# Kernel tuning notes

Measured on AMD Instinct MI355X. Metric: run time of the kernel, lower is better.

The kernel has to match this reference:

```python
import jax, jax.numpy as jnp
import numpy as np
from jax import lax

DG = 8  # deformable groups


def conv3(x, w, b):
    # 3x3 stride-1 SAME conv, NCHW/OIHW
    y = lax.conv_general_dilated(x, w, (1, 1), 'SAME',
                                 dimension_numbers=('NCHW', 'OIHW', 'NCHW'))
    return y + b[None, :, None, None]


def lrelu(x):
    return jnp.where(x >= 0, x, 0.1 * x)


def _mdcn(x, offset, mask, w, b, dg):
    """Modulated deformable conv v2: 3x3, stride 1, pad 1, dilation 1, groups 1.
    offset: [B, 2*dg*9, H, W] (first dg*9 = y offsets, second dg*9 = x offsets),
    mask:   [B, dg*9, H, W] (already sigmoided)."""
    B, C, H, W = x.shape
    kk = 9
    Cg = C // dg
    off = offset.reshape(B, 2, dg, kk, H, W)
    oy, ox = off[:, 0], off[:, 1]            # [B, dg, kk, H, W]
    m = mask.reshape(B, dg, kk, H, W)
    ky = (jnp.arange(kk) // 3 - 1).astype(x.dtype).reshape(1, 1, kk, 1, 1)
    kx = (jnp.arange(kk) % 3 - 1).astype(x.dtype).reshape(1, 1, kk, 1, 1)
    hg = jnp.arange(H, dtype=x.dtype).reshape(1, 1, 1, H, 1)
    wg = jnp.arange(W, dtype=x.dtype).reshape(1, 1, 1, 1, W)
    py = hg + ky + oy                        # sampling positions (pad=1 cancels k-1 shift)
    px = wg + kx + ox
    y0 = jnp.floor(py)
    x0 = jnp.floor(px)
    wy = py - y0
    wx = px - x0
    xg = x.reshape(B, dg, Cg, H * W)
    acc = jnp.zeros((B, dg, Cg, kk, H, W), x.dtype)
    for dy, dx, wgt in ((0.0, 0.0, (1 - wy) * (1 - wx)),
                        (0.0, 1.0, (1 - wy) * wx),
                        (1.0, 0.0, wy * (1 - wx)),
                        (1.0, 1.0, wy * wx)):
        yy = y0 + dy
        xx = x0 + dx
        valid = (yy >= 0) & (yy < H) & (xx >= 0) & (xx < W)
        yi = jnp.clip(yy, 0, H - 1).astype(jnp.int32)
        xi = jnp.clip(xx, 0, W - 1).astype(jnp.int32)
        idx = (yi * W + xi).reshape(B, dg, 1, kk * H * W)
        v = jnp.take_along_axis(xg, idx, axis=3).reshape(B, dg, Cg, kk, H, W)
        acc = acc + v * (wgt * valid.astype(x.dtype))[:, :, None]
    acc = acc * m[:, :, None]                # modulation mask
    sampled = acc.reshape(B, C, kk, H, W)
    out = jnp.einsum('bckhw,ock->bohw', sampled, w.reshape(w.shape[0], C, kk))
    return out + b[None, :, None, None]


def _dcn_pack(x, feat, w_om, b_om, w, b):
    out = conv3(feat, w_om, b_om)            # [B, 3*dg*9, H, W]
    o1, o2, mr = jnp.split(out, 3, axis=1)
    offset = jnp.concatenate([o1, o2], axis=1)
    mask = jax.nn.sigmoid(mr)
    return _mdcn(x, offset, mask, w, b, DG)


def _forward(ref, neb,
             w_oc1, b_oc1, w_om1, b_om1, w_dcn1, b_dcn1, w_fc, b_fc,
             w_cas1, b_cas1, w_cas2, b_cas2, w_om2, b_om2, w_dcn2, b_dcn2,
             w_ta1, b_ta1, w_ta2, b_ta2, w_ff, b_ff):
    start = ref
    # --- PCD alignment (nbr_feat_l = neb, ref_feat_l = ref) ---
    off = lrelu(conv3(jnp.concatenate([neb, ref], axis=1), w_oc1, b_oc1))
    feat = _dcn_pack(neb, off, w_om1, b_om1, w_dcn1, b_dcn1)
    feat = lrelu(conv3(feat, w_fc, b_fc))
    off = jnp.concatenate([feat, ref], axis=1)
    off = lrelu(conv3(lrelu(conv3(off, w_cas1, b_cas1)), w_cas2, b_cas2))
    feat = lrelu(_dcn_pack(feat, off, w_om2, b_om2, w_dcn2, b_dcn2))
    # --- TSA fusion (ref=ref, neb=feat) ---
    emb_ref = conv3(ref, w_ta1, b_ta1)
    emb = conv3(feat, w_ta2, b_ta2)
    corr = jnp.sum(emb * emb_ref, axis=1, keepdims=True)  # [B,1,H,W]
    feat = lrelu(conv3(ref * corr, w_ff, b_ff))
    return feat + start


def setup_inputs() -> dict:
    key = jax.random.key(0)
    ks = jax.random.split(key, 32)
    B, C, H, W = 4, 64, 180, 320
    s = 0.05
    p = lambda k, shape: (jax.random.normal(k, shape, jnp.float32) * s)
    OM = 3 * DG * 9  # 216
    return {
        'ref': jax.random.normal(ks[0], (B, C, H, W), jnp.float32),
        'neb': jax.random.normal(ks[1], (B, C, H, W), jnp.float32),
        'w_oc1': p(ks[2], (C, 2 * C, 3, 3)), 'b_oc1': p(ks[3], (C,)),
        'w_om1': p(ks[4], (OM, C, 3, 3)),    'b_om1': p(ks[5], (OM,)),
        'w_dcn1': p(ks[6], (C, C, 3, 3)),    'b_dcn1': p(ks[7], (C,)),
        'w_fc': p(ks[8], (C, C, 3, 3)),      'b_fc': p(ks[9], (C,)),
        'w_cas1': p(ks[10], (C, 2 * C, 3, 3)), 'b_cas1': p(ks[11], (C,)),
        'w_cas2': p(ks[12], (C, C, 3, 3)),   'b_cas2': p(ks[13], (C,)),
        'w_om2': p(ks[14], (OM, C, 3, 3)),   'b_om2': p(ks[15], (OM,)),
        'w_dcn2': p(ks[16], (C, C, 3, 3)),   'b_dcn2': p(ks[17], (C,)),
        'w_ta1': p(ks[18], (C, C, 3, 3)),    'b_ta1': p(ks[19], (C,)),
        'w_ta2': p(ks[20], (C, C, 3, 3)),    'b_ta2': p(ks[21], (C,)),
        'w_ff': p(ks[22], (C, C, 3, 3)),     'b_ff': p(ks[23], (C,)),
    }


def reference(ref, neb,
              w_oc1, b_oc1, w_om1, b_om1, w_dcn1, b_dcn1, w_fc, b_fc,
              w_cas1, b_cas1, w_cas2, b_cas2, w_om2, b_om2, w_dcn2, b_dcn2,
              w_ta1, b_ta1, w_ta2, b_ta2, w_ff, b_ff):
    return _forward(ref, neb,
                    w_oc1, b_oc1, w_om1, b_om1, w_dcn1, b_dcn1, w_fc, b_fc,
                    w_cas1, b_cas1, w_cas2, b_cas2, w_om2, b_om2, w_dcn2, b_dcn2,
                    w_ta1, b_ta1, w_ta2, b_ta2, w_ff, b_ff)
```

## Files before the change

### kernel.cpp

```cpp
#include <hip/hip_runtime.h>
#include <cmath>


using short8 = __attribute__((ext_vector_type(8))) short;
using f32x4  = __attribute__((ext_vector_type(4))) float;
using f32x2  = __attribute__((ext_vector_type(2))) float;

#define DEVINL static __device__ __forceinline__

DEVINL unsigned short f2bf(float f){
    unsigned u = __float_as_uint(f);
    u += 0x7fffu + ((u >> 16) & 1u);
    return (unsigned short)(u >> 16);
}
DEVINL unsigned pack2(float a, float b){ return (unsigned)f2bf(a) | ((unsigned)f2bf(b) << 16); }
DEVINL float bflo(unsigned u){ return __uint_as_float(u << 16); }
DEVINL float bfhi(unsigned u){ return __uint_as_float(u & 0xffff0000u); }
DEVINL float bf2f(unsigned short u){ return __uint_as_float((unsigned)u << 16); }
DEVINL float lrelu_f(float v){ return v >= 0.f ? v : 0.1f * v; }
DEVINL f32x2 up2(unsigned u){
    return f32x2{__uint_as_float(u << 16), __uint_as_float(u & 0xffff0000u)};
}

DEVINL void swz_decode(int& bx, int& by, int& bz){
    const int gx = gridDim.x, gy = gridDim.y;
    int lin = blockIdx.x + gx * (blockIdx.y + gy * blockIdx.z);
    int nwg = gx * gy * gridDim.z;
    int q = nwg >> 3, r = nwg & 7;
    int xcd = lin & 7, idx = lin >> 3;
    int swz = (xcd < r ? xcd * (q + 1) : r + xcd * q) + idx;
    bz = swz / (gx * gy);
    int rem = swz - bz * gx * gy;
    by = rem / gx; bx = rem - by * gx;
}

struct Ptr4 { unsigned short* p[4]; };

__global__ __launch_bounds__(256) void nchw2nhwc2(const float* __restrict__ inA,
                                                  const float* __restrict__ inB,
                                                  unsigned short* __restrict__ outA,
                                                  unsigned short* __restrict__ outB)
{
    constexpr int HW = 180 * 320;
    const int blk = blockIdx.x;
    const float* in = (blk < 900) ? inA : inB;
    unsigned short* out = (blk < 900) ? outA : outB;
    size_t idx = (size_t)(blk % 900) * 256 + threadIdx.x;
    size_t bb = idx / HW, p = idx % HW;
    const float* src = in + (bb * 64) * (size_t)HW + p;
    unsigned short* dst = out + idx * 64;
    #pragma unroll
    for (int c0 = 0; c0 < 64; c0 += 16) {
        unsigned r[8];
        #pragma unroll
        for (int q = 0; q < 8; ++q)
            r[q] = pack2(src[(size_t)(c0 + 2*q) * HW], src[(size_t)(c0 + 2*q + 1) * HW]);
        *(uint4*)(dst + c0)     = *(uint4*)&r[0];
        *(uint4*)(dst + c0 + 8) = *(uint4*)&r[4];
    }
}

struct PrepArgs {
    const float* src[11];
    unsigned short* dst[11];
    int cout[11]; int cin[11]; int nch[11]; int kind[11];
};

__global__ __launch_bounds__(256) void prep_all(PrepArgs a)
{
    const int t = blockIdx.y;
    const int idx = blockIdx.x * 256 + threadIdx.x;
    if (a.kind[t] == 1) {
        if (idx >= 36864) return;
        int kk = idx & 31, oc = (idx >> 5) & 63, s = idx >> 11;
        int k = s * 32 + kk;
        int gt = k >> 3, c8 = k & 7;
        int tap = gt >> 3, g = gt & 7;
        a.dst[t][idx] = f2bf(a.src[t][((size_t)oc * 64 + g * 8 + c8) * 9 + tap]);
    } else {
        int cin = a.cin[t], cout = a.cout[t];
        int ncs = cin / 32;
        int total = a.nch[t] * 9 * ncs * 2048;
        if (idx >= total) return;
        int kk = idx & 31, oc_l = (idx >> 5) & 63, rest = idx >> 11;
        int cs = rest % ncs; int rest2 = rest / ncs;
        int j = rest2 % 9; int ch = rest2 / 9;
        int oc = ch * 64 + oc_l, c = cs * 32 + kk;
        float v = (oc < cout) ? a.src[t][((size_t)oc * cin + c) * 9 + j] : 0.f;
        a.dst[t][idx] = f2bf(v);
    }
}

template<int CIN, bool TWO_IN, bool ACT, bool SCALE, int OUTMODE, int NM, int NF>
__global__ __launch_bounds__(256, (CIN == 128 ? 2 : 3)) void conv_mfma(
    const unsigned short* __restrict__ in0, const unsigned short* __restrict__ in1,
    const unsigned short* __restrict__ wgt, const float* __restrict__ bias,
    unsigned short* __restrict__ out, const float* __restrict__ corr,
    const float* __restrict__ res, float* __restrict__ outf,
    Ptr4 omout, int choff, int zdiv, int COUT)
{
    constexpr int H = 180, W = 320, HW = H * W;
    constexpr int NCB = CIN / 8;
    constexpr int NCS = CIN / 32;
    constexpr int XW  = NF * 16 + 2;
    __shared__ __align__(16) unsigned char lds[6 * XW * CIN * 2];

    const int tid = threadIdx.x;
    int bx, by, bz;
    swz_decode(bx, by, bz);
    int b, ch;
    if (OUTMODE == 1) { b = bz / zdiv; ch = bz % zdiv + choff; }
    else              { b = bz; ch = 0; }
    const int x0 = bx * (NF * 16), y0 = by * 4;

    for (int t = tid; t < 6 * XW * NCB; t += 256) {
        int cb = t % NCB; int r = t / NCB;
        int xp = r % XW, yp = r / XW;
        int gx = x0 - 1 + xp, gy = y0 - 1 + yp;
        uint4 v = make_uint4(0, 0, 0, 0);
        if (gx >= 0 && gx < W && gy >= 0 && gy < H) {
            size_t pix = (size_t)b * HW + (size_t)gy * W + gx;
            const unsigned short* src;
            if (TWO_IN) src = (cb < 8) ? (in0 + pix * 64 + cb * 8) : (in1 + pix * 64 + (cb - 8) * 8);
            else        src = in0 + pix * CIN + cb * 8;
            v = *(const uint4*)src;
            if (SCALE) {
                float cv = corr[pix];
                v.x = pack2(bflo(v.x) * cv, bfhi(v.x) * cv);
                v.y = pack2(bflo(v.y) * cv, bfhi(v.y) * cv);
                v.z = pack2(bflo(v.z) * cv, bfhi(v.z) * cv);
                v.w = pack2(bflo(v.w) * cv, bfhi(v.w) * cv);
            }
        }
        int blk = cb ^ (xp & 7);
        *(uint4*)&lds[(size_t)((yp * XW + xp) * NCB + blk) * 16] = v;
    }
    __syncthreads();

    const int wv = tid >> 6, lane = tid & 63;
    const int ll = lane & 15, lh = lane >> 4;
    const unsigned short* wchunk = wgt + (size_t)ch * (9 * NCS * 2048);
    const int alane = ll * 32 + lh * 8;

    f32x4 acc[NM][NF];
    #pragma unroll
    for (int mi = 0; mi < NM; ++mi)
        #pragma unroll
        for (int nf = 0; nf < NF; ++nf) acc[mi][nf] = f32x4{0.f, 0.f, 0.f, 0.f};

    #pragma unroll
    for (int j = 0; j < 9; ++j) {
        const int jy = j / 3, jx = j % 3;
        #pragma unroll
        for (int cs = 0; cs < NCS; ++cs) {
            const int s = j * NCS + cs;
            short8 a[NM];
            #pragma unroll
            for (int mi = 0; mi < NM; ++mi)
                a[mi] = *(const short8*)(wchunk + (size_t)s * 2048 + mi * 512 + alane);
            short8 bf[NF];
            #pragma unroll
            for (int nf = 0; nf < NF; ++nf) {
                int xp = nf * 16 + ll + jx;
                int blk = (cs * 4 + lh) ^ (xp & 7);
                int addr = (((wv + jy) * XW + xp) * NCB + blk) * 16;
                bf[nf] = *(const short8*)&lds[addr];
            }
            #pragma unroll
            for (int mi = 0; mi < NM; ++mi)
                #pragma unroll
                for (int nf = 0; nf < NF; ++nf)
                    acc[mi][nf] = __builtin_amdgcn_mfma_f32_16x16x32_bf16(a[mi], bf[nf], acc[mi][nf], 0, 0, 0);
        }
    }

    const int py = y0 + wv;
    const size_t pixrow = (size_t)b * HW + (size_t)py * W;
    #pragma unroll
    for (int nf = 0; nf < NF; ++nf) {
        const int px = x0 + nf * 16 + ll;
        if (OUTMODE == 1) {
            unsigned short* oslot = omout.p[b];
            #pragma unroll
            for (int mi = 0; mi < NM; ++mi) {
                const int oc_l = mi * 16 + lh * 4;
                #pragma unroll
                for (int jj = 0; jj < 4; ++jj) {
                    int ocg = ch * 64 + oc_l + jj;
                    if (ocg < COUT) {
                        float t = acc[mi][nf][jj] + bias[ocg];
                        oslot[(size_t)ocg * HW + (size_t)py * W + px] = f2bf(ACT ? lrelu_f(t) : t);
                    }
                }
            }
        } else {
            #pragma unroll
            for (int mi = 0; mi < NM; ++mi) {
                const int oc_l = mi * 16 + lh * 4;
                if (OUTMODE == 0) {
                    float v[4];
                    #pragma unroll
                    for (int jj = 0; jj < 4; ++jj) {
                        float t = acc[mi][nf][jj] + bias[oc_l + jj];
                        v[jj] = ACT ? lrelu_f(t) : t;
                    }
                    uint2 st; st.x = pack2(v[0], v[1]); st.y = pack2(v[2], v[3]);
                    *(uint2*)&out[(pixrow + px) * 64 + oc_l] = st;
                } else {
                    #pragma unroll
                    for (int jj = 0; jj < 4; ++jj) {
                        int oc = oc_l + jj;
                        float t = acc[mi][nf][jj] + bias[oc];
                        if (ACT) t = lrelu_f(t);
                        size_t idx = ((size_t)b * 64 + oc) * HW + (size_t)py * W + px;
                        outf[idx] = t + res[idx];
                    }
                }
            }
        }
    }
}

__global__ __launch_bounds__(256, 3) void tacorr_mfma(
    const unsigned short* __restrict__ inR,
    const unsigned short* __restrict__ inE,
    const unsigned short* __restrict__ wR, const float* __restrict__ bR,
    const unsigned short* __restrict__ wE, const float* __restrict__ bE,
    float* __restrict__ outf)
{
    constexpr int H = 180, W = 320, HW = H * W;
    constexpr int NE1 = 6 * 34 * 8;
    __shared__ __align__(16) unsigned char lds[2][6 * 34 * 64 * 2];

    const int tid = threadIdx.x;
    int bx, by, bz;
    swz_decode(bx, by, bz);
    const int b = bz;
    const int x0 = bx * 32, y0 = by * 4;

    for (int t = tid; t < 2 * NE1; t += 256) {
        int half = t / NE1, e = t - half * NE1;
        int cb = e & 7; int r = e >> 3;
        int xp = r % 34, yp = r / 34;
        int gx = x0 - 1 + xp, gy = y0 - 1 + yp;
        uint4 v = make_uint4(0, 0, 0, 0);
        if (gx >= 0 && gx < W && gy >= 0 && gy < H) {
            size_t pix = (size_t)b * HW + (size_t)gy * W + gx;
            const unsigned short* src = (half ? inE : inR) + pix * 64 + cb * 8;
            v = *(const uint4*)src;
        }
        int blk = cb ^ (xp & 7);
        *(uint4*)&lds[half][(size_t)((yp * 34 + xp) * 8 + blk) * 16] = v;
    }
    __syncthreads();

    const int wv = tid >> 6, lane = tid & 63;
    const int ll = lane & 15, lh = lane >> 4;
    const int alane = ll * 32 + lh * 8;

    f32x4 accR[4][2], accE[4][2];
    #pragma unroll
    for (int mi = 0; mi < 4; ++mi)
        #pragma unroll
        for (int nf = 0; nf < 2; ++nf) { accR[mi][nf] = f32x4{0,0,0,0}; accE[mi][nf] = f32x4{0,0,0,0}; }

    #pragma unroll
    for (int j = 0; j < 9; ++j) {
        const int jy = j / 3, jx = j % 3;
        #pragma unroll
        for (int cs = 0; cs < 2; ++cs) {
            const int s = j * 2 + cs;
            short8 aR[4], aE[4];
            #pragma unroll
            for (int mi = 0; mi < 4; ++mi) {
                aR[mi] = *(const short8*)(wR + (size_t)s * 2048 + mi * 512 + alane);
                aE[mi] = *(const short8*)(wE + (size_t)s * 2048 + mi * 512 + alane);
            }
            #pragma unroll
            for (int nf = 0; nf < 2; ++nf) {
                int xp = nf * 16 + ll + jx;
                int blk = (cs * 4 + lh) ^ (xp & 7);
                int addr = (((wv + jy) * 34 + xp) * 8 + blk) * 16;
                short8 bfR = *(const short8*)&lds[0][addr];
                short8 bfE = *(const short8*)&lds[1][addr];
                #pragma unroll
                for (int mi = 0; mi < 4; ++mi) {
                    accR[mi][nf] = __builtin_amdgcn_mfma_f32_16x16x32_bf16(aR[mi], bfR, accR[mi][nf], 0, 0, 0);
                    accE[mi][nf] = __builtin_amdgcn_mfma_f32_16x16x32_bf16(aE[mi], bfE, accE[mi][nf], 0, 0, 0);
                }
            }
        }
    }

    const int py = y0 + wv;
    const size_t pixrow = (size_t)b * HW + (size_t)py * W;
    #pragma unroll
    for (int nf = 0; nf < 2; ++nf) {
        const int px = x0 + nf * 16 + ll;
        float dot = 0.f;
        #pragma unroll
        for (int mi = 0; mi < 4; ++mi) {
            const int oc_l = mi * 16 + lh * 4;
            #pragma unroll
            for (int jj = 0; jj < 4; ++jj)
                dot += (accR[mi][nf][jj] + bR[oc_l + jj]) * (accE[mi][nf][jj] + bE[oc_l + jj]);
        }
        dot += __shfl_xor(dot, 16);
        dot += __shfl_xor(dot, 32);
        if (lh == 0) outf[pixrow + px] = dot;
    }
}

template<int ACT>
__global__ __launch_bounds__(256, 6) void mdcn_mfma(
    const unsigned short* __restrict__ x, Ptr4 omslots,
    const unsigned short* __restrict__ wgt, const float* __restrict__ bias,
    unsigned short* __restrict__ out)
{
    constexpr int H = 180, W = 320, HW = H * W;
    constexpr size_t CHW = (size_t)HW * 64;
    __shared__ __align__(16) unsigned char sv[40 * 32 * 16];

    const int tid = threadIdx.x;
    int bx, by, bz;
    swz_decode(bx, by, bz);
    const unsigned short* xb  = x + (size_t)bz * CHW;
    const unsigned short* omb = omslots.p[bz];
    unsigned short* ob        = out + (size_t)bz * CHW;
    const int px0 = bx * 32;
    const int py  = by;

    const int pxl = tid & 31, g = tid >> 5;
    const int px = px0 + pxl;
    const size_t p = (size_t)py * W + px;
    const unsigned short* omg = omb + (size_t)(g * 9) * HW + p;

    float oyv[9], oxv[9], mmv[9];
    #pragma unroll
    for (int k = 0; k < 9; ++k) oyv[k] = bf2f(omg[(size_t)k * HW]);
    #pragma unroll
    for (int k = 0; k < 9; ++k) oxv[k] = bf2f(omg[(size_t)(72 + k) * HW]);
    #pragma unroll
    for (int k = 0; k < 9; ++k) mmv[k] = bf2f(omg[(size_t)(144 + k) * HW]);

    auto SAMPLE = [&](int k, int row){
        float m = 1.f / (1.f + __expf(-mmv[k]));
        float pyf = (float)(py + (k / 3) - 1) + oyv[k];
        float pxf = (float)(px + (k % 3) - 1) + oxv[k];
        float y0f = floorf(pyf), x0f = floorf(pxf);
        float wy = pyf - y0f, wx = pxf - x0f;
        int yi = (int)y0f, xi = (int)x0f;
        bool vy0 = (yi >= 0) && (yi < H);
        bool vy1 = (yi + 1 >= 0) && (yi + 1 < H);
        bool vx0 = (xi >= 0) && (xi < W);
        bool vx1 = (xi + 1 >= 0) && (xi + 1 < W);
        float w00 = (vy0 && vx0) ? (1.f - wy) * (1.f - wx) * m : 0.f;
        float w01 = (vy0 && vx1) ? (1.f - wy) * wx * m : 0.f;
        float w10 = (vy1 && vx0) ? wy * (1.f - wx) * m : 0.f;
        float w11 = (vy1 && vx1) ? wy * wx * m : 0.f;
        int yc0 = min(max(yi, 0), H - 1), yc1 = min(max(yi + 1, 0), H - 1);
        int xc0 = min(max(xi, 0), W - 1), xc1 = min(max(xi + 1, 0), W - 1);
        uint4 c00 = *(const uint4*)(xb + ((size_t)(yc0 * W + xc0) * 64 + g * 8));
        uint4 c01 = *(const uint4*)(xb + ((size_t)(yc0 * W + xc1) * 64 + g * 8));
        uint4 c10 = *(const uint4*)(xb + ((size_t)(yc1 * W + xc0) * 64 + g * 8));
        uint4 c11 = *(const uint4*)(xb + ((size_t)(yc1 * W + xc1) * 64 + g * 8));
        const unsigned* p00 = (const unsigned*)&c00;
        const unsigned* p01 = (const unsigned*)&c01;
        const unsigned* p10 = (const unsigned*)&c10;
        const unsigned* p11 = (const unsigned*)&c11;
        unsigned r[4];
        #pragma unroll
        for (int q = 0; q < 4; ++q) {
            f32x2 rv = up2(p00[q]) * w00 + up2(p01[q]) * w01
                     + up2(p10[q]) * w10 + up2(p11[q]) * w11;
            r[q] = pack2(rv[0], rv[1]);
        }
        *(uint4*)&sv[(size_t)(row * 32 + pxl) * 16] = *(uint4*)r;
    };

    const int wv = tid >> 6, lane = tid & 63;
    const int ll = lane & 15, lh = lane >> 4;
    f32x4 acc[2] = {f32x4{0.f,0.f,0.f,0.f}, f32x4{0.f,0.f,0.f,0.f}};

    #pragma unroll
    for (int k = 0; k < 5; ++k) SAMPLE(k, k * 8 + g);
    __syncthreads();
    #pragma unroll
    for (int s = 0; s < 10; ++s) {
        short8 a = *(const short8*)(wgt + (size_t)(s * 64 + wv * 16 + ll) * 32 + lh * 8);
        #pragma unroll
        for (int nf = 0; nf < 2; ++nf) {
            short8 bb = *(const short8*)&sv[(size_t)s * 2048 + lh * 512 + (nf * 16 + ll) * 16];
            acc[nf] = __builtin_amdgcn_mfma_f32_16x16x32_bf16(a, bb, acc[nf], 0, 0, 0);
        }
    }
    __syncthreads();
    #pragma unroll
    for (int k = 5; k < 9; ++k) SAMPLE(k, (k - 5) * 8 + g);
    __syncthreads();
    #pragma unroll
    for (int s = 0; s < 8; ++s) {
        short8 a = *(const short8*)(wgt + (size_t)((10 + s) * 64 + wv * 16 + ll) * 32 + lh * 8);
        #pragma unroll
        for (int nf = 0; nf < 2; ++nf) {
            short8 bb = *(const short8*)&sv[(size_t)s * 2048 + lh * 512 + (nf * 16 + ll) * 16];
            acc[nf] = __builtin_amdgcn_mfma_f32_16x16x32_bf16(a, bb, acc[nf], 0, 0, 0);
        }
    }

    #pragma unroll
    for (int nf = 0; nf < 2; ++nf) {
        int opx = px0 + nf * 16 + ll;
        int oc0 = wv * 16 + lh * 4;
        float v[4];
        #pragma unroll
        for (int jj = 0; jj < 4; ++jj) {
            float t = acc[nf][jj] + bias[oc0 + jj];
            v[jj] = ACT ? lrelu_f(t) : t;
        }
        uint2 st; st.x = pack2(v[0], v[1]); st.y = pack2(v[2], v[3]);
        *(uint2*)&ob[((size_t)py * W + opx) * 64 + oc0] = st;
    }
}

extern "C" void kernel_launch(void* const* d_in, const int* in_sizes, int n_in,
                              void* d_out, int out_size, void* d_ws, size_t ws_size,
                              hipStream_t stream)
{
    const float* ref    = (const float*)d_in[0];
    const float* neb    = (const float*)d_in[1];
    const float* w_oc1  = (const float*)d_in[2];  const float* b_oc1  = (const float*)d_in[3];
    const float* w_om1  = (const float*)d_in[4];  const float* b_om1  = (const float*)d_in[5];
    const float* w_dcn1 = (const float*)d_in[6];  const float* b_dcn1 = (const float*)d_in[7];
    const float* w_fc   = (const float*)d_in[8];  const float* b_fc   = (const float*)d_in[9];
    const float* w_cas1 = (const float*)d_in[10]; const float* b_cas1 = (const float*)d_in[11];
    const float* w_cas2 = (const float*)d_in[12]; const float* b_cas2 = (const float*)d_in[13];
    const float* w_om2  = (const float*)d_in[14]; const float* b_om2  = (const float*)d_in[15];
    const float* w_dcn2 = (const float*)d_in[16]; const float* b_dcn2 = (const float*)d_in[17];
    const float* w_ta1  = (const float*)d_in[18]; const float* b_ta1  = (const float*)d_in[19];
    const float* w_ta2  = (const float*)d_in[20]; const float* b_ta2  = (const float*)d_in[21];
    const float* w_ff   = (const float*)d_in[22]; const float* b_ff   = (const float*)d_in[23];

    constexpr int H = 180, W = 320, HW = H * W;
    constexpr size_t CHW = (size_t)HW * 64;
    constexpr size_t SLB = 4 * CHW * 2;
    constexpr size_t OMSLOT_EL = (size_t)HW * 216;
    constexpr size_t OMSLOT_B  = OMSLOT_EL * 2;

    char* wsb = (char*)d_ws;
    unsigned short* S0 = (unsigned short*)(wsb);
    unsigned short* S1 = (unsigned short*)(wsb + SLB);
    unsigned short* S2 = (unsigned short*)(wsb + 2 * SLB);
    unsigned short* S3 = (unsigned short*)(wsb + 3 * SLB);
    float* corrf = (float*)S3;
    unsigned short* ffw = (unsigned short*)(wsb + SLB + (2u << 20));

    char* doutb = (char*)d_out;
    unsigned short* omA0 = (unsigned short*)doutb;
    unsigned short* omA1 = omA0 + OMSLOT_EL;
    unsigned short* wb   = (unsigned short*)(doutb + 2 * OMSLOT_B);
    const bool big = ws_size >= 4 * SLB + 2 * OMSLOT_B;
    unsigned short* omB0 = (unsigned short*)(wsb + 4 * SLB);
    unsigned short* omB1 = omB0 + OMSLOT_EL;

    unsigned short* w_oc1p = wb + 0;
    unsigned short* w_om1p = wb + 73728;
    unsigned short* w_dcn1p= wb + 221184;
    unsigned short* w_fcp  = wb + 258048;
    unsigned short* w_cas1p= wb + 294912;
    unsigned short* w_cas2p= wb + 368640;
    unsigned short* w_om2p = wb + 405504;
    unsigned short* w_dcn2p= wb + 552960;
    unsigned short* w_ta1p = wb + 589824;
    unsigned short* w_ta2p = wb + 626688;
    unsigned short* w_ffp  = wb + 663552;

    dim3 blk(256);
    dim3 g4(10, 45, 4);
    dim3 g4w(5, 45, 4);
    Ptr4 none{};

    nchw2nhwc2<<<1800, blk, 0, stream>>>(ref, neb, S0, S1);

    {
        PrepArgs pa;
        const float* srcs[11] = {w_oc1, w_om1, w_dcn1, w_fc, w_cas1, w_cas2, w_om2, w_dcn2, w_ta1, w_ta2, w_ff};
        unsigned short* dsts[11] = {w_oc1p, w_om1p, w_dcn1p, w_fcp, w_cas1p, w_cas2p, w_om2p, w_dcn2p, w_ta1p, w_ta2p, w_ffp};
        int couts[11] = {64, 216, 0, 64, 64, 64, 216, 0, 64, 64, 64};
        int cins[11]  = {128, 64, 0, 64, 128, 64, 64, 0, 64, 64, 64};
        int nchs[11]  = {1, 4, 0, 1, 1, 1, 4, 0, 1, 1, 1};
        int kinds[11] = {0, 0, 1, 0, 0, 0, 0, 1, 0, 0, 0};
        for (int i = 0; i < 11; ++i) {
            pa.src[i] = srcs[i]; pa.dst[i] = dsts[i];
            pa.cout[i] = couts[i]; pa.cin[i] = cins[i]; pa.nch[i] = nchs[i]; pa.kind[i] = kinds[i];
        }
        prep_all<<<dim3(576, 11), blk, 0, stream>>>(pa);
    }

    conv_mfma<128, true, true, false, 0, 4, 2><<<g4, blk, 0, stream>>>(
        S1, S0, w_oc1p, b_oc1, S2, nullptr, nullptr, nullptr, none, 0, 1, 64);

    auto ompack = [&](const unsigned short* inp, const unsigned short* wp, const float* bp,
                      Ptr4 slots, int nb){
        conv_mfma<64, false, false, false, 1, 4, 4><<<dim3(5, 45, 3 * nb), blk, 0, stream>>>(
            inp, nullptr, wp, bp, nullptr, nullptr, nullptr, nullptr, slots, 0, 3, 216);
        conv_mfma<64, false, false, false, 1, 2, 4><<<dim3(5, 45, nb), blk, 0, stream>>>(
            inp, nullptr, wp, bp, nullptr, nullptr, nullptr, nullptr, slots, 3, 1, 216);
    };

    if (big) {
        Ptr4 slots{omA0, omA1, omB0, omB1};
        ompack(S2, w_om1p, b_om1, slots, 4);
        mdcn_mfma<0><<<dim3(10, 180, 4), blk, 0, stream>>>(S1, slots, w_dcn1p, b_dcn1, S3);
    } else {
        Ptr4 slots{omA0, omA1, nullptr, nullptr};
        for (int pp = 0; pp < 2; ++pp) {
            ompack(S2 + 2 * pp * CHW, w_om1p, b_om1, slots, 2);
            mdcn_mfma<0><<<dim3(10, 180, 2), blk, 0, stream>>>(S1 + 2 * pp * CHW, slots,
                                                               w_dcn1p, b_dcn1, S3 + 2 * pp * CHW);
        }
    }

    conv_mfma<64, false, true, false, 0, 4, 4><<<g4w, blk, 0, stream>>>(
        S3, nullptr, w_fcp, b_fc, S2, nullptr, nullptr, nullptr, none, 0, 1, 64);
    conv_mfma<128, true, true, false, 0, 4, 2><<<g4, blk, 0, stream>>>(
        S2, S0, w_cas1p, b_cas1, S1, nullptr, nullptr, nullptr, none, 0, 1, 64);
    conv_mfma<64, false, true, false, 0, 4, 4><<<g4w, blk, 0, stream>>>(
        S1, nullptr, w_cas2p, b_cas2, S3, nullptr, nullptr, nullptr, none, 0, 1, 64);

    if (big) {
        Ptr4 slots{omA0, omA1, omB0, omB1};
        ompack(S3, w_om2p, b_om2, slots, 4);
        mdcn_mfma<1><<<dim3(10, 180, 4), blk, 0, stream>>>(S2, slots, w_dcn2p, b_dcn2, S1);
    } else {
        Ptr4 slots{omA0, omA1, nullptr, nullptr};
        for (int pp = 0; pp < 2; ++pp) {
            ompack(S3 + 2 * pp * CHW, w_om2p, b_om2, slots, 2);
            mdcn_mfma<1><<<dim3(10, 180, 2), blk, 0, stream>>>(S2 + 2 * pp * CHW, slots,
                                                               w_dcn2p, b_dcn2, S1 + 2 * pp * CHW);
        }
    }

    tacorr_mfma<<<g4, blk, 0, stream>>>(S0, S1, w_ta1p, b_ta1, w_ta2p, b_ta2, corrf);

    hipMemcpyAsync(ffw, w_ffp, 36864 * 2, hipMemcpyDeviceToDevice, stream);

    conv_mfma<64, false, true, true, 2, 4, 4><<<g4w, blk, 0, stream>>>(
        S0, nullptr, ffw, b_ff, nullptr, corrf, ref, (float*)d_out, none, 0, 1, 64);
}
```

Before: 1.161 ms.

## Double mdcn block to 512 threads, sampling all nine taps in one phase

The deformable-conv kernel now runs 512 threads per block. The two halves of the block sample taps 0-4 and 5-8 at the same time into a larger shared buffer (72 rows instead of 40), with a single barrier before the MFMA phase. Each of the 8 waves then computes one 16x16 output tile over all 18 K-steps, instead of 4 waves each doing two tiles in two phases. This removes two barriers and the serial sample-compute-sample sequence and exposes more gather parallelism. In exchange it uses more LDS per block and tighter register limits under launch_bounds(512,8), which may reduce the number of resident blocks.

```diff
diff --git a/kernel.cpp b/kernel.cpp
--- a/kernel.cpp
+++ b/kernel.cpp
@@ -312,14 +312,14 @@
 }
 
 template<int ACT>
-__global__ __launch_bounds__(256, 6) void mdcn_mfma(
+__global__ __launch_bounds__(512, 8) void mdcn_mfma(
     const unsigned short* __restrict__ x, Ptr4 omslots,
     const unsigned short* __restrict__ wgt, const float* __restrict__ bias,
     unsigned short* __restrict__ out)
 {
     constexpr int H = 180, W = 320, HW = H * W;
     constexpr size_t CHW = (size_t)HW * 64;
-    __shared__ __align__(16) unsigned char sv[40 * 32 * 16];
+    __shared__ __align__(16) unsigned char sv[72 * 32 * 16];
 
     const int tid = threadIdx.x;
     int bx, by, bz;
@@ -330,23 +330,15 @@
     const int px0 = bx * 32;
     const int py  = by;
 
-    const int pxl = tid & 31, g = tid >> 5;
+    const int pxl = tid & 31, g = (tid >> 5) & 7, hh = tid >> 8;
     const int px = px0 + pxl;
     const size_t p = (size_t)py * W + px;
     const unsigned short* omg = omb + (size_t)(g * 9) * HW + p;
 
-    float oyv[9], oxv[9], mmv[9];
-    #pragma unroll
-    for (int k = 0; k < 9; ++k) oyv[k] = bf2f(omg[(size_t)k * HW]);
-    #pragma unroll
-    for (int k = 0; k < 9; ++k) oxv[k] = bf2f(omg[(size_t)(72 + k) * HW]);
-    #pragma unroll
-    for (int k = 0; k < 9; ++k) mmv[k] = bf2f(omg[(size_t)(144 + k) * HW]);
-
-    auto SAMPLE = [&](int k, int row){
-        float m = 1.f / (1.f + __expf(-mmv[k]));
-        float pyf = (float)(py + (k / 3) - 1) + oyv[k];
-        float pxf = (float)(px + (k % 3) - 1) + oxv[k];
+    auto SAMPLE = [&](int k, float oy, float ox, float mr){
+        float m = 1.f / (1.f + __expf(-mr));
+        float pyf = (float)(py + (k / 3) - 1) + oy;
+        float pxf = (float)(px + (k % 3) - 1) + ox;
         float y0f = floorf(pyf), x0f = floorf(pxf);
         float wy = pyf - y0f, wx = pxf - x0f;
         int yi = (int)y0f, xi = (int)x0f;
@@ -375,47 +367,50 @@
                      + up2(p10[q]) * w10 + up2(p11[q]) * w11;
             r[q] = pack2(rv[0], rv[1]);
         }
-        *(uint4*)&sv[(size_t)(row * 32 + pxl) * 16] = *(uint4*)r;
+        *(uint4*)&sv[(size_t)((k * 8 + g) * 32 + pxl) * 16] = *(uint4*)r;
     };
+
+    if (hh == 0) {
+        float oy[5], ox[5], mr[5];
+        #pragma unroll
+        for (int k = 0; k < 5; ++k) oy[k] = bf2f(omg[(size_t)k * HW]);
+        #pragma unroll
+        for (int k = 0; k < 5; ++k) ox[k] = bf2f(omg[(size_t)(72 + k) * HW]);
+        #pragma unroll
+        for (int k = 0; k < 5; ++k) mr[k] = bf2f(omg[(size_t)(144 + k) * HW]);
+        #pragma unroll
+        for (int k = 0; k < 5; ++k) SAMPLE(k, oy[k], ox[k], mr[k]);
+    } else {
+        float oy[4], ox[4], mr[4];
+        #pragma unroll
+        for (int k = 0; k < 4; ++k) oy[k] = bf2f(omg[(size_t)(5 + k) * HW]);
+        #pragma unroll
+        for (int k = 0; k < 4; ++k) ox[k] = bf2f(omg[(size_t)(77 + k) * HW]);
+        #pragma unroll
+        for (int k = 0; k < 4; ++k) mr[k] = bf2f(omg[(size_t)(149 + k) * HW]);
+        #pragma unroll
+        for (int k = 0; k < 4; ++k) SAMPLE(5 + k, oy[k], ox[k], mr[k]);
+    }
+    __syncthreads();
 
     const int wv = tid >> 6, lane = tid & 63;
     const int ll = lane & 15, lh = lane >> 4;
-    f32x4 acc[2] = {f32x4{0.f,0.f,0.f,0.f}, f32x4{0.f,0.f,0.f,0.f}};
-
-    #pragma unroll
-    for (int k = 0; k < 5; ++k) SAMPLE(k, k * 8 + g);
-    __syncthreads();
-    #pragma unroll
-    for (int s = 0; s < 10; ++s) {
-        short8 a = *(const short8*)(wgt + (size_t)(s * 64 + wv * 16 + ll) * 32 + lh * 8);
-        #pragma unroll
-        for (int nf = 0; nf < 2; ++nf) {
-            short8 bb = *(const short8*)&sv[(size_t)s * 2048 + lh * 512 + (nf * 16 + ll) * 16];
-            acc[nf] = __builtin_amdgcn_mfma_f32_16x16x32_bf16(a, bb, acc[nf], 0, 0, 0);
-        }
-    }
-    __syncthreads();
-    #pragma unroll
-    for (int k = 5; k < 9; ++k) SAMPLE(k, (k - 5) * 8 + g);
-    __syncthreads();
-    #pragma unroll
-    for (int s = 0; s < 8; ++s) {
-        short8 a = *(const short8*)(wgt + (size_t)((10 + s) * 64 + wv * 16 + ll) * 32 + lh * 8);
-        #pragma unroll
-        for (int nf = 0; nf < 2; ++nf) {
-            short8 bb = *(const short8*)&sv[(size_t)s * 2048 + lh * 512 + (nf * 16 + ll) * 16];
-            acc[nf] = __builtin_amdgcn_mfma_f32_16x16x32_bf16(a, bb, acc[nf], 0, 0, 0);
-        }
-    }
-
-    #pragma unroll
-    for (int nf = 0; nf < 2; ++nf) {
+    const int og = wv & 3, nf = wv >> 2;
+    f32x4 acc = f32x4{0.f, 0.f, 0.f, 0.f};
+    #pragma unroll
+    for (int s = 0; s < 18; ++s) {
+        short8 a = *(const short8*)(wgt + (size_t)(s * 64 + og * 16 + ll) * 32 + lh * 8);
+        short8 bb = *(const short8*)&sv[(size_t)s * 2048 + lh * 512 + (nf * 16 + ll) * 16];
+        acc = __builtin_amdgcn_mfma_f32_16x16x32_bf16(a, bb, acc, 0, 0, 0);
+    }
+
+    {
         int opx = px0 + nf * 16 + ll;
-        int oc0 = wv * 16 + lh * 4;
+        int oc0 = og * 16 + lh * 4;
         float v[4];
         #pragma unroll
         for (int jj = 0; jj < 4; ++jj) {
-            float t = acc[nf][jj] + bias[oc0 + jj];
+            float t = acc[jj] + bias[oc0 + jj];
             v[jj] = ACT ? lrelu_f(t) : t;
         }
         uint2 st; st.x = pack2(v[0], v[1]); st.y = pack2(v[2], v[3]);
@@ -476,6 +471,7 @@
     unsigned short* w_ffp  = wb + 663552;
 
     dim3 blk(256);
+    dim3 blk512(512);
     dim3 g4(10, 45, 4);
     dim3 g4w(5, 45, 4);
     Ptr4 none{};
@@ -511,13 +507,13 @@
     if (big) {
         Ptr4 slots{omA0, omA1, omB0, omB1};
         ompack(S2, w_om1p, b_om1, slots, 4);
-        mdcn_mfma<0><<<dim3(10, 180, 4), blk, 0, stream>>>(S1, slots, w_dcn1p, b_dcn1, S3);
+        mdcn_mfma<0><<<dim3(10, 180, 4), blk512, 0, stream>>>(S1, slots, w_dcn1p, b_dcn1, S3);
     } else {
         Ptr4 slots{omA0, omA1, nullptr, nullptr};
         for (int pp = 0; pp < 2; ++pp) {
             ompack(S2 + 2 * pp * CHW, w_om1p, b_om1, slots, 2);
-            mdcn_mfma<0><<<dim3(10, 180, 2), blk, 0, stream>>>(S1 + 2 * pp * CHW, slots,
-                                                               w_dcn1p, b_dcn1, S3 + 2 * pp * CHW);
+            mdcn_mfma<0><<<dim3(10, 180, 2), blk512, 0, stream>>>(S1 + 2 * pp * CHW, slots,
+                                                                  w_dcn1p, b_dcn1, S3 + 2 * pp * CHW);
         }
     }
 
@@ -531,13 +527,13 @@
     if (big) {
         Ptr4 slots{omA0, omA1, omB0, omB1};
         ompack(S3, w_om2p, b_om2, slots, 4);
-        mdcn_mfma<1><<<dim3(10, 180, 4), blk, 0, stream>>>(S2, slots, w_dcn2p, b_dcn2, S1);
+        mdcn_mfma<1><<<dim3(10, 180, 4), blk512, 0, stream>>>(S2, slots, w_dcn2p, b_dcn2, S1);
     } else {
         Ptr4 slots{omA0, omA1, nullptr, nullptr};
         for (int pp = 0; pp < 2; ++pp) {
             ompack(S3 + 2 * pp * CHW, w_om2p, b_om2, slots, 2);
-            mdcn_mfma<1><<<dim3(10, 180, 2), blk, 0, stream>>>(S2 + 2 * pp * CHW, slots,
-                                                               w_dcn2p, b_dcn2, S1 + 2 * pp * CHW);
+            mdcn_mfma<1><<<dim3(10, 180, 2), blk512, 0, stream>>>(S2 + 2 * pp * CHW, slots,
+                                                                  w_dcn2p, b_dcn2, S1 + 2 * pp * CHW);
         }
     }
 
```

Result: slower. 1.192 ms (+2.6%).
